# Kernel tuning notes

Hardware: AMD Instinct MI355X
Metric: run time of the kernel (lower is better)

Reference implementation:

```python
import jax, jax.numpy as jnp
import numpy as np


def setup_inputs() -> dict:
    key = jax.random.key(0)
    k1, k2, k3 = jax.random.split(key, 3)
    N, C_in, H, W = 16, 64, 256, 256
    C_out, K = 128, 3
    x = jax.random.normal(k1, (N, C_in, H, W), dtype=jnp.float32)
    # kaiming-ish small init for stability through tanh
    conv_weight = jax.random.normal(k2, (C_out, C_in, K, K), dtype=jnp.float32) * 0.05
    conv_bias = jax.random.normal(k3, (C_out,), dtype=jnp.float32) * 0.05
    return {"x": x, "conv_weight": conv_weight, "conv_bias": conv_bias}


def reference(x, conv_weight, conv_bias):
    # VALID conv, stride 1, NCHW / OIHW (matches the CUDA kernel: H_out = H - K + 1)
    y = jax.lax.conv_general_dilated(
        x, conv_weight,
        window_strides=(1, 1), padding='VALID',
        dimension_numbers=('NCHW', 'OIHW', 'NCHW'))
    y = y + conv_bias[None, :, None, None]
    # fused pattern: double tanh then per-pixel min over output channels (keepdim)
    y = jnp.tanh(jnp.tanh(y))
    out = jnp.min(y, axis=1, keepdims=True)  # (N, 1, H_out, W_out)
    return out
```

## Files before the change

kernel.cpp:

```cpp
#include <hip/hip_runtime.h>
#include <stdint.h>

typedef _Float16 half8 __attribute__((ext_vector_type(8)));
typedef float float4v __attribute__((ext_vector_type(4)));

#define H_IN 256
#define W_IN 256
#define H_OUT 254
#define W_OUT 254
#define T_COLS 68
#define A_ROWS 408
#define A_BYTES (A_ROWS * 128)
#define B_BYTES (2 * 8192)
#define MIN_BYTES (2 * 256 * 4)
#define SMEM_BYTES (A_BYTES + B_BYTES + MIN_BYTES)

__global__ void pack_w_kernel(const float* __restrict__ w, _Float16* __restrict__ Bp3) {
    int idx = blockIdx.x * 256 + threadIdx.x;
    if (idx >= 73728) return;
    int g   = idx >> 12;
    int rem = idx & 4095;
    int co  = rem >> 5;
    int s16 = (rem >> 3) & 3;
    int e   = rem & 7;
    int q   = s16 ^ (co & 3);
    int tap = g >> 1, h = g & 1;
    int cin = h * 32 + q * 8 + e;
    int kh  = tap / 3, kw = tap - kh * 3;
    Bp3[idx] = (_Float16)w[(co * 64 + cin) * 9 + kh * 3 + kw];
}

__device__ __forceinline__ int akey(int row) {
    return (((row & 7) ^ ((row >> 3) & 7)) << 4);
}

__global__ __launch_bounds__(512, 4)
void conv_v7_kernel(const float* __restrict__ x,
                    const _Float16* __restrict__ Bp3,
                    const float* __restrict__ bias,
                    float* __restrict__ out) {
    extern __shared__ __align__(16) char smem[];
    char*  Alds   = smem;
    char*  Blds   = smem + A_BYTES;
    float* minbuf = (float*)(smem + A_BYTES + B_BYTES);

    const int tid  = threadIdx.x;
    const int lane = tid & 63;
    const int wave = tid >> 6;
    const int ow0  = blockIdx.x * 64;
    const int oh0  = blockIdx.y * 4;
    const int nb   = blockIdx.z;
    const int wr   = wave >> 1;
    const int wc   = wave & 1;
    const int q    = lane >> 4;
    const int lr   = lane & 15;

    {
        const char* src = (const char*)Bp3 + tid * 16;
        char* dstb = Blds + (tid & ~63) * 16;
        __builtin_amdgcn_global_load_lds(
            (const __attribute__((address_space(1))) uint32_t*)src,
            (__attribute__((address_space(3))) uint32_t*)dstb, 16, 0, 0);
    }

    {
        const float* xb = x + (size_t)nb * (64 * H_IN * W_IN);
#pragma unroll
        for (int k = 0; k < 2; ++k) {
            int id = tid + 512 * k;
            if (id < 816) {
                int oct  = (unsigned)id / 102u;
                int pxq  = id - oct * 102;
                int row0 = pxq * 4;
                int r    = (unsigned)row0 / (unsigned)T_COLS;
                int c    = row0 - r * T_COLS;
                int ih   = oh0 + r; if (ih > H_IN - 1) ih = H_IN - 1;
                int iw   = ow0 + c; if (iw > W_IN - 4) iw = W_IN - 4;
                const float* src = xb + (size_t)(oct * 8) * (H_IN * W_IN)
                                      + (size_t)ih * W_IN + iw;
                float4v f[8];
#pragma unroll
                for (int u = 0; u < 8; ++u)
                    f[u] = *(const float4v*)(src + (size_t)u * (H_IN * W_IN));
#pragma unroll
                for (int j = 0; j < 4; ++j) {
                    int row = row0 + j;
                    half8 hv;
#pragma unroll
                    for (int u = 0; u < 8; ++u) hv[u] = (_Float16)f[u][j];
                    *(half8*)(Alds + row * 128 + ((oct * 16) ^ akey(row))) = hv;
                }
            }
        }
    }

    float bv[4];
#pragma unroll
    for (int n = 0; n < 4; ++n) bv[n] = bias[wc * 64 + n * 16 + lr];

    float4v acc[4][4];
#pragma unroll
    for (int m = 0; m < 4; ++m)
#pragma unroll
        for (int n = 0; n < 4; ++n)
#pragma unroll
            for (int i = 0; i < 4; ++i) acc[m][n][i] = 0.0f;

    const int bslot = (q ^ (lr & 3)) << 4;
    const int bco   = (wc * 64 + lr) * 64;

#pragma unroll
    for (int g = 0; g < 18; ++g) {
        __syncthreads();

        if (g < 17) {
            const char* src = (const char*)Bp3 + (size_t)(g + 1) * 8192 + tid * 16;
            char* dstb = Blds + ((g + 1) & 1) * 8192 + (tid & ~63) * 16;
            __builtin_amdgcn_global_load_lds(
                (const __attribute__((address_space(1))) uint32_t*)src,
                (__attribute__((address_space(3))) uint32_t*)dstb, 16, 0, 0);
        }

        const int tap = g >> 1, h = g & 1;
        const int kh = tap / 3, kw = tap - kh * 3;
        const int kb = h * 64 + q * 16;

        half8 a[4], b[4];
#pragma unroll
        for (int n = 0; n < 4; ++n)
            b[n] = *(const half8*)(Blds + (g & 1) * 8192 + bco + n * 1024 + bslot);
#pragma unroll
        for (int m = 0; m < 4; ++m) {
            int row = (wr + kh) * T_COLS + m * 16 + lr + kw;
            a[m] = *(const half8*)(Alds + row * 128 + (kb ^ akey(row)));
        }
#pragma unroll
        for (int m = 0; m < 4; ++m)
#pragma unroll
            for (int n = 0; n < 4; ++n)
                acc[m][n] = __builtin_amdgcn_mfma_f32_16x16x32_f16(
                    a[m], b[n], acc[m][n], 0, 0, 0);
    }

#pragma unroll
    for (int m = 0; m < 4; ++m) {
        float4v v;
#pragma unroll
        for (int n = 0; n < 4; ++n) {
#pragma unroll
            for (int i = 0; i < 4; ++i) {
                float t = acc[m][n][i] + bv[n];
                v[i] = (n == 0) ? t : fminf(v[i], t);
            }
        }
#pragma unroll
        for (int off = 1; off < 16; off <<= 1)
#pragma unroll
            for (int i = 0; i < 4; ++i)
                v[i] = fminf(v[i], __shfl_xor(v[i], off, 64));
        if (lr == 0) {
#pragma unroll
            for (int i = 0; i < 4; ++i)
                minbuf[wc * 256 + wr * 64 + m * 16 + q * 4 + i] = v[i];
        }
    }
    __syncthreads();

    if (tid < 256) {
        int r = tid >> 6, c = tid & 63;
        int oh = oh0 + r, ow = ow0 + c;
        if (oh < H_OUT && ow < W_OUT) {
            float mv = fminf(minbuf[tid], minbuf[256 + tid]);
            out[((size_t)nb * H_OUT + oh) * W_OUT + ow] = tanhf(tanhf(mv));
        }
    }
}

extern "C" void kernel_launch(void* const* d_in, const int* in_sizes, int n_in,
                              void* d_out, int out_size, void* d_ws, size_t ws_size,
                              hipStream_t stream) {
    const float* x    = (const float*)d_in[0];
    const float* w    = (const float*)d_in[1];
    const float* bias = (const float*)d_in[2];
    float* out        = (float*)d_out;
    _Float16* Bp3     = (_Float16*)d_ws;

    pack_w_kernel<<<dim3(288), dim3(256), 0, stream>>>(w, Bp3);
    conv_v7_kernel<<<dim3(4, 64, 16), dim3(512), SMEM_BYTES, stream>>>(x, Bp3, bias, out);
}
```

Measured before the change: 175.6 us.

## Triple-buffer weight slabs with vmcnt-based waits and MFMA priority boost

```diff
diff --git a/kernel.cpp b/kernel.cpp
--- a/kernel.cpp
+++ b/kernel.cpp
@@ -11,7 +11,8 @@
 #define T_COLS 68
 #define A_ROWS 408
 #define A_BYTES (A_ROWS * 128)
-#define B_BYTES (2 * 8192)
+#define B_SLAB  8192
+#define B_BYTES (3 * B_SLAB)
 #define MIN_BYTES (2 * 256 * 4)
 #define SMEM_BYTES (A_BYTES + B_BYTES + MIN_BYTES)
 
@@ -23,7 +24,7 @@
     int co  = rem >> 5;
     int s16 = (rem >> 3) & 3;
     int e   = rem & 7;
-    int q   = s16 ^ (co & 3);
+    int q   = s16 ^ ((co >> 2) & 3);
     int tap = g >> 1, h = g & 1;
     int cin = h * 32 + q * 8 + e;
     int kh  = tap / 3, kw = tap - kh * 3;
@@ -35,7 +36,7 @@
 }
 
 __global__ __launch_bounds__(512, 4)
-void conv_v7_kernel(const float* __restrict__ x,
+void conv_v8_kernel(const float* __restrict__ x,
                     const _Float16* __restrict__ Bp3,
                     const float* __restrict__ bias,
                     float* __restrict__ out) {
@@ -55,13 +56,18 @@
     const int q    = lane >> 4;
     const int lr   = lane & 15;
 
-    {
-        const char* src = (const char*)Bp3 + tid * 16;
-        char* dstb = Blds + (tid & ~63) * 16;
+#pragma unroll
+    for (int s = 0; s < 2; ++s) {
+        const char* src = (const char*)Bp3 + s * B_SLAB + tid * 16;
+        char* dstb = Blds + s * B_SLAB + (tid & ~63) * 16;
         __builtin_amdgcn_global_load_lds(
             (const __attribute__((address_space(1))) uint32_t*)src,
             (__attribute__((address_space(3))) uint32_t*)dstb, 16, 0, 0);
     }
+
+    float bv[4];
+#pragma unroll
+    for (int n = 0; n < 4; ++n) bv[n] = bias[wc * 64 + n * 16 + lr];
 
     {
         const float* xb = x + (size_t)nb * (64 * H_IN * W_IN);
@@ -93,10 +99,7 @@
             }
         }
     }
-
-    float bv[4];
-#pragma unroll
-    for (int n = 0; n < 4; ++n) bv[n] = bias[wc * 64 + n * 16 + lr];
+    __syncthreads();
 
     float4v acc[4][4];
 #pragma unroll
@@ -106,16 +109,19 @@
 #pragma unroll
             for (int i = 0; i < 4; ++i) acc[m][n][i] = 0.0f;
 
-    const int bslot = (q ^ (lr & 3)) << 4;
+    const int bslot = (q ^ ((lr >> 2) & 3)) << 4;
     const int bco   = (wc * 64 + lr) * 64;
 
 #pragma unroll
     for (int g = 0; g < 18; ++g) {
-        __syncthreads();
+        if (g < 17) asm volatile("s_waitcnt vmcnt(1)" ::: "memory");
+        else        asm volatile("s_waitcnt vmcnt(0)" ::: "memory");
+        __builtin_amdgcn_s_barrier();
+        __builtin_amdgcn_sched_barrier(0);
 
-        if (g < 17) {
-            const char* src = (const char*)Bp3 + (size_t)(g + 1) * 8192 + tid * 16;
-            char* dstb = Blds + ((g + 1) & 1) * 8192 + (tid & ~63) * 16;
+        if (g < 16) {
+            const char* src = (const char*)Bp3 + (size_t)(g + 2) * B_SLAB + tid * 16;
+            char* dstb = Blds + ((g + 2) % 3) * B_SLAB + (tid & ~63) * 16;
             __builtin_amdgcn_global_load_lds(
                 (const __attribute__((address_space(1))) uint32_t*)src,
                 (__attribute__((address_space(3))) uint32_t*)dstb, 16, 0, 0);
@@ -128,18 +134,21 @@
         half8 a[4], b[4];
 #pragma unroll
         for (int n = 0; n < 4; ++n)
-            b[n] = *(const half8*)(Blds + (g & 1) * 8192 + bco + n * 1024 + bslot);
+            b[n] = *(const half8*)(Blds + (g % 3) * B_SLAB + bco + n * 1024 + bslot);
 #pragma unroll
         for (int m = 0; m < 4; ++m) {
             int row = (wr + kh) * T_COLS + m * 16 + lr + kw;
             a[m] = *(const half8*)(Alds + row * 128 + (kb ^ akey(row)));
         }
+
+        __builtin_amdgcn_s_setprio(1);
 #pragma unroll
         for (int m = 0; m < 4; ++m)
 #pragma unroll
             for (int n = 0; n < 4; ++n)
                 acc[m][n] = __builtin_amdgcn_mfma_f32_16x16x32_f16(
                     a[m], b[n], acc[m][n], 0, 0, 0);
+        __builtin_amdgcn_s_setprio(0);
     }
 
 #pragma unroll
@@ -186,5 +195,5 @@
     _Float16* Bp3     = (_Float16*)d_ws;
 
     pack_w_kernel<<<dim3(288), dim3(256), 0, stream>>>(w, Bp3);
-    conv_v7_kernel<<<dim3(4, 64, 16), dim3(512), SMEM_BYTES, stream>>>(x, Bp3, bias, out);
+    conv_v8_kernel<<<dim3(4, 64, 16), dim3(512), SMEM_BYTES, stream>>>(x, Bp3, bias, out);
 }
```

Result: faster. 168.6 us (-4.0%).
